# Kernel tuning notes

Measured on AMD Instinct MI355X. Metric: run time of the kernel, lower is better.

## Reference

```python
import jax, jax.numpy as jnp
import numpy as np

B, G, GS = 1024, 2000, 25   # batch, num gene groups, group size
H1, H2, C = 1024, 512, 10
EPS = 1e-5


def _xavier(key, shape, fan_in, fan_out):
    lim = np.sqrt(6.0 / (fan_in + fan_out))
    return jax.random.uniform(key, shape, jnp.float32, -lim, lim)


def setup_inputs() -> dict:
    key = jax.random.key(0)
    ks = jax.random.split(key, 8)
    x = jax.random.normal(ks[0], (B, G * GS), jnp.float32)
    # per-group Linear(GS, 1) weights stacked -> block-diagonal grouped GEMM
    gene_w = _xavier(ks[1], (G, GS), GS, 1)
    gene_b = jnp.zeros((G,), jnp.float32)
    W1 = _xavier(ks[2], (G, H1), G, H1)
    b1 = jnp.zeros((H1,), jnp.float32)
    W2 = _xavier(ks[3], (H1, H2), H1, H2)
    b2 = jnp.zeros((H2,), jnp.float32)
    Wout = _xavier(ks[4], (H2, C), H2, C)
    bout = jnp.zeros((C,), jnp.float32)
    Wres = _xavier(ks[5], (G, C), G, C)
    bres = jnp.zeros((C,), jnp.float32)
    gamma1 = jnp.ones((H1,), jnp.float32); beta1 = jnp.zeros((H1,), jnp.float32)
    gamma2 = jnp.ones((H2,), jnp.float32); beta2 = jnp.zeros((H2,), jnp.float32)
    return dict(x=x, gene_w=gene_w, gene_b=gene_b, W1=W1, b1=b1,
                gamma1=gamma1, beta1=beta1, W2=W2, b2=b2,
                gamma2=gamma2, beta2=beta2, Wout=Wout, bout=bout,
                Wres=Wres, bres=bres)


def _batch_norm(h, gamma, beta):
    # training-mode BatchNorm1d: biased batch statistics over axis 0
    mu = jnp.mean(h, axis=0)
    var = jnp.mean(jnp.square(h - mu), axis=0)
    return gamma * (h - mu) * jax.lax.rsqrt(var + EPS) + beta


def reference(x, gene_w, gene_b, W1, b1, gamma1, beta1, W2, b2,
              gamma2, beta2, Wout, bout, Wres, bres):
    # fused replacement for the per-group Linear(GS,1)+ReLU loop + cat
    xg = x.reshape(B, G, GS)
    g = jax.nn.relu(jnp.einsum('bgk,gk->bg', xg, gene_w) + gene_b)  # [B, G]
    h1 = jax.nn.relu(_batch_norm(g @ W1 + b1, gamma1, beta1))       # [B, H1]
    h2 = jax.nn.relu(_batch_norm(h1 @ W2 + b2, gamma2, beta2))      # [B, H2]
    x_main = h2 @ Wout + bout                                       # [B, C]
    x_res = g @ Wres + bres                                         # [B, C]
    return jax.nn.softmax(x_main + x_res, axis=1)
```

## Files before the change

kernel.cpp:

```cpp
#include <hip/hip_runtime.h>
#include <math.h>

#define NB   1024
#define NG   2000
#define NGS  25
#define KP   2048
#define NH1  1024
#define NH2  512
#define NC   10
#define EPSV 1e-5f
#define GPB  200
#define RB   8


typedef __attribute__((ext_vector_type(8)))  __bf16 bf16x8;
typedef __attribute__((ext_vector_type(4)))  float  f32x4;
typedef __attribute__((ext_vector_type(16))) float  f32x16;
typedef __attribute__((ext_vector_type(8)))  unsigned short u16x8;
typedef __attribute__((ext_vector_type(4)))  unsigned short u16x4;

__device__ __forceinline__ unsigned short f2bf(float f) {
  union { float f; unsigned u; } v; v.f = f;
  return (unsigned short)((v.u + 0x7fffu + ((v.u >> 16) & 1u)) >> 16);
}
__device__ __forceinline__ float bf2f(unsigned short b) {
  union { unsigned u; float f; } v; v.u = ((unsigned)b) << 16;
  return v.f;
}

__global__ __launch_bounds__(256) void prep_kernel(
    const float* __restrict__ x, const float* __restrict__ gw,
    const float* __restrict__ gb, unsigned short* __restrict__ g_bf,
    const float* __restrict__ W1, unsigned short* __restrict__ W1bT,
    const float* __restrict__ W2, unsigned short* __restrict__ W2bT,
    const float* __restrict__ Wres, float* __restrict__ rp,
    float* __restrict__ stats) {
  __shared__ __attribute__((aligned(16))) float xs[GPB * NGS];
  __shared__ __attribute__((aligned(16))) float ws[GPB * NC];
  __shared__ float rred[4][NC];
  int t = threadIdx.x;

  if (blockIdx.y < 10) {
    int blk = blockIdx.y;
    int b0 = blockIdx.x * RB;
    const float4* gsrc = (const float4*)(gw + (size_t)blk * (GPB * NGS));
    float4* xd = (float4*)xs;
    for (int i = t; i < (GPB * NGS) / 4; i += 256) xd[i] = gsrc[i];
    const float4* wsrc = (const float4*)(Wres + (size_t)blk * (GPB * NC));
    float4* wd = (float4*)ws;
    for (int i = t; i < (GPB * NC) / 4; i += 256) wd[i] = wsrc[i];
    __syncthreads();
    float gwr[NGS];
    float gbv = 0.f;
    int gi = blk * GPB + t;
    if (t < GPB) {
#pragma unroll
      for (int k = 0; k < NGS; ++k) gwr[k] = xs[t * NGS + k];
      gbv = gb[gi];
    }
    __syncthreads();
    int lane = t & 63, wave = t >> 6;
    for (int r = 0; r < RB; ++r) {
      int b = b0 + r;
      const float4* src = (const float4*)(x + (size_t)b * (NG * NGS) + blk * (GPB * NGS));
      for (int i = t; i < (GPB * NGS) / 4; i += 256) xd[i] = src[i];
      __syncthreads();
      float g = 0.f;
      if (t < GPB) {
        float acc = 0.f;
        const float* xp = xs + t * NGS;
#pragma unroll
        for (int k = 0; k < NGS; ++k) acc = fmaf(xp[k], gwr[k], acc);
        g = fmaxf(acc + gbv, 0.f);
        g_bf[(size_t)b * KP + gi] = f2bf(g);
      } else if (blk == 9 && t < GPB + (KP - NG)) {
        g_bf[(size_t)b * KP + NG + (t - GPB)] = 0;
      }
#pragma unroll
      for (int c = 0; c < NC; ++c) {
        float v = (t < GPB) ? g * ws[t * NC + c] : 0.f;
        for (int off = 32; off > 0; off >>= 1) v += __shfl_down(v, off, 64);
        if (lane == 0) rred[wave][c] = v;
      }
      __syncthreads();
      if (t < NC)
        rp[(size_t)b * (10 * NC) + blk * NC + t] =
            rred[0][t] + rred[1][t] + rred[2][t] + rred[3][t];
      __syncthreads();
    }
    return;
  }

  int px = (blockIdx.y - 10) * 128 + blockIdx.x;
  if (px == 640) {
    for (int i = t; i < 3072; i += 256) stats[i] = 0.f;
    return;
  }
  if (px > 640) return;
  const float* src; unsigned short* dst; int K, N, Kpad, k0, n0;
  if (px < 512)      { src = W1; dst = W1bT; K = NG;  N = NH1; Kpad = KP;
                       k0 = (px & 31) * 64; n0 = (px >> 5) * 64; }
  else               { int xi = px - 512;
                       src = W2; dst = W2bT; K = NH1; N = NH2; Kpad = NH1;
                       k0 = (xi & 15) * 64; n0 = (xi >> 4) * 64; }

  unsigned short (*ts)[72] = (unsigned short (*)[72])xs;
  int c4 = (t & 15) * 4;
  int r  = t >> 4;
  for (int rr = r; rr < 64; rr += 16) {
    int k = k0 + rr;
    float4 v = make_float4(0.f, 0.f, 0.f, 0.f);
    if (k < K) v = *(const float4*)&src[(size_t)k * N + n0 + c4];
    ts[rr][c4 + 0] = f2bf(v.x); ts[rr][c4 + 1] = f2bf(v.y);
    ts[rr][c4 + 2] = f2bf(v.z); ts[rr][c4 + 3] = f2bf(v.w);
  }
  __syncthreads();
  int rr8 = (t & 7) * 8;
  int cc  = t >> 3;
  for (int c = cc; c < 64; c += 32) {
    u16x8 val;
#pragma unroll
    for (int i = 0; i < 8; ++i) val[i] = ts[rr8 + i][c];
    *(u16x8*)&dst[(size_t)(n0 + c) * Kpad + k0 + rr8] = val;
  }
}

__global__ __launch_bounds__(256) void gemm1_kernel(
    const unsigned short* __restrict__ A,
    const unsigned short* __restrict__ Bt,
    float* __restrict__ C, float* __restrict__ sum, float* __restrict__ sq,
    int M, int N, int Kp) {
  __shared__ unsigned short As[32][68];
  __shared__ unsigned short Bs[64][68];
  __shared__ float ebuf[2 * 64 * 17];
  int t = threadIdx.x;
  int m0 = blockIdx.y * 32, n0 = blockIdx.x * 64;
  int wave = t >> 6, lane = t & 63;
  int h = wave & 1;
  int p = wave >> 1;
  int l31 = lane & 31, l5 = lane >> 5;
  int srow = t >> 3, skc = (t & 7) * 8;

  f32x16 acc;
#pragma unroll
  for (int q = 0; q < 16; ++q) acc[q] = 0.f;

  const unsigned short* Ap = A + (size_t)(m0 + srow) * Kp + skc;
  const unsigned short* Bp = Bt + (size_t)(n0 + srow) * Kp + skc;
  size_t rstep = 32 * (size_t)Kp;

  u16x8 pa0 = *(const u16x8*)(Ap);
  u16x8 pb0 = *(const u16x8*)(Bp);
  u16x8 pb1 = *(const u16x8*)(Bp + rstep);

  for (int k0 = 0; k0 < Kp; k0 += 64) {
    *(u16x8*)&As[srow][skc]      = pa0;
    *(u16x8*)&Bs[srow][skc]      = pb0;
    *(u16x8*)&Bs[srow + 32][skc] = pb1;
    __syncthreads();
    if (k0 + 64 < Kp) {
      pa0 = *(const u16x8*)(Ap + k0 + 64);
      pb0 = *(const u16x8*)(Bp + k0 + 64);
      pb1 = *(const u16x8*)(Bp + k0 + 64 + rstep);
    }
    int kb = p * 32 + l5 * 8;
    {
      bf16x8 av = *(const bf16x8*)&As[l31][kb];
      bf16x8 bv = *(const bf16x8*)&Bs[h * 32 + l31][kb];
      acc = __builtin_amdgcn_mfma_f32_32x32x16_bf16(av, bv, acc, 0, 0, 0);
    }
    {
      bf16x8 av = *(const bf16x8*)&As[l31][kb + 16];
      bf16x8 bv = *(const bf16x8*)&Bs[h * 32 + l31][kb + 16];
      acc = __builtin_amdgcn_mfma_f32_32x32x16_bf16(av, bv, acc, 0, 0, 0);
    }
    __syncthreads();
  }

  float* eb = ebuf + (size_t)(h * 64 + lane) * 17;
  if (p == 1) {
#pragma unroll
    for (int r = 0; r < 16; ++r) eb[r] = acc[r];
  }
  __syncthreads();
  if (p == 0) {
    float s = 0.f, ss = 0.f;
#pragma unroll
    for (int r = 0; r < 16; ++r) {
      float v = acc[r] + eb[r];
      int row = m0 + (r & 3) + 8 * (r >> 2) + 4 * l5;
      C[(size_t)row * N + n0 + h * 32 + l31] = v;
      s += v;
      ss = fmaf(v, v, ss);
    }
    s  += __shfl_down(s, 32, 64);
    ss += __shfl_down(ss, 32, 64);
    if (lane < 32) {
      atomicAdd(&sum[n0 + h * 32 + lane], s);
      atomicAdd(&sq[n0 + h * 32 + lane], ss);
    }
  }
}

__global__ __launch_bounds__(256) void gemm2_kernel(
    const float* __restrict__ A,
    const unsigned short* __restrict__ Bt,
    float* __restrict__ C, const float* __restrict__ sum1,
    const float* __restrict__ sq1, const float* __restrict__ gam1,
    const float* __restrict__ bet1, float* __restrict__ sum2,
    float* __restrict__ sq2, int M, int N, int Kp) {
  __shared__ unsigned short As[32][72];
  __shared__ unsigned short Bs[32][72];
  __shared__ float sc1s[NH1], sh1s[NH1];
  int t = threadIdx.x;
  int m0 = blockIdx.y * 32, n0 = blockIdx.x * 32;
  int wave = t >> 6, lane = t & 63;
  int wm = (wave >> 1) * 16, wn = (wave & 1) * 16;
  int fm = lane & 15, fk = (lane >> 4) * 8;
  int srow = t >> 3, skc = (t & 7) * 8;

  for (int k = t; k < Kp; k += 256) {
    float mu  = sum1[k] * (1.f / NB);
    float var = sq1[k] * (1.f / NB) - mu * mu;
    float scv = gam1[k] * rsqrtf(var + EPSV);
    sc1s[k] = scv;
    sh1s[k] = fmaf(-mu, scv, bet1[k]);
  }

  f32x4 acc = (f32x4){0.f, 0.f, 0.f, 0.f};

  const float* Ap = A + (size_t)(m0 + srow) * Kp + skc;
  const unsigned short* Bp = Bt + (size_t)(n0 + srow) * Kp + skc;

  f32x4 pa0 = *(const f32x4*)(Ap);
  f32x4 pa1 = *(const f32x4*)(Ap + 4);
  u16x8 pb0 = *(const u16x8*)(Bp);
  __syncthreads();

  for (int k0 = 0; k0 < Kp; k0 += 64) {
    f32x4 scl = *(const f32x4*)&sc1s[k0 + skc];
    f32x4 sch = *(const f32x4*)&sc1s[k0 + skc + 4];
    f32x4 shl = *(const f32x4*)&sh1s[k0 + skc];
    f32x4 shh = *(const f32x4*)&sh1s[k0 + skc + 4];
    u16x8 a0;
#pragma unroll
    for (int i = 0; i < 4; ++i) {
      a0[i]     = f2bf(fmaxf(fmaf(pa0[i], scl[i], shl[i]), 0.f));
      a0[i + 4] = f2bf(fmaxf(fmaf(pa1[i], sch[i], shh[i]), 0.f));
    }
    *(u16x8*)&As[srow][skc] = a0;
    *(u16x8*)&Bs[srow][skc] = pb0;
    __syncthreads();
    if (k0 + 64 < Kp) {
      pa0 = *(const f32x4*)(Ap + k0 + 64);
      pa1 = *(const f32x4*)(Ap + k0 + 64 + 4);
      pb0 = *(const u16x8*)(Bp + k0 + 64);
    }
#pragma unroll
    for (int s = 0; s < 2; ++s) {
      bf16x8 af = *(const bf16x8*)&As[wm + fm][s * 32 + fk];
      bf16x8 bf = *(const bf16x8*)&Bs[wn + fm][s * 32 + fk];
      acc = __builtin_amdgcn_mfma_f32_16x16x32_bf16(af, bf, acc, 0, 0, 0);
    }
    __syncthreads();
  }

  int crow = (lane >> 4) * 4, ccol = lane & 15;
  float s = 0.f, ss = 0.f;
#pragma unroll
  for (int r = 0; r < 4; ++r) {
    float v = acc[r];
    int m = m0 + wm + crow + r;
    int n = n0 + wn + ccol;
    C[(size_t)m * N + n] = v;
    s += v;
    ss = fmaf(v, v, ss);
  }
  s  += __shfl_down(s, 32, 64);  s  += __shfl_down(s, 16, 64);
  ss += __shfl_down(ss, 32, 64); ss += __shfl_down(ss, 16, 64);
  if (lane < 16) {
    atomicAdd(&sum2[n0 + wn + lane], s);
    atomicAdd(&sq2[n0 + wn + lane], ss);
  }
}

__global__ __launch_bounds__(256) void final_kernel(
    const float* __restrict__ t2, const float* __restrict__ sum2,
    const float* __restrict__ sq2, const float* __restrict__ gam2,
    const float* __restrict__ bet2, const float* __restrict__ rp,
    const float* __restrict__ Wout, const float* __restrict__ bout,
    const float* __restrict__ bres, float* __restrict__ out) {
  __shared__ __attribute__((aligned(16))) float wl[NH2 * NC];
  __shared__ float red[4][NC];
  __shared__ float logits[NC];
  int b = blockIdx.x;
  int t = threadIdx.x;

  const float4* wsrc = (const float4*)Wout;
  float4* wdst = (float4*)wl;
#pragma unroll
  for (int i = 0; i < (NH2 * NC / 4) / 256; ++i)
    wdst[t + i * 256] = wsrc[t + i * 256];
  __syncthreads();

  float acc[NC] = {};
#pragma unroll
  for (int half = 0; half < 2; ++half) {
    int h = t + half * 256;
    float raw = t2[(size_t)b * NH2 + h];
    float mu  = sum2[h] * (1.f / NB);
    float var = sq2[h] * (1.f / NB) - mu * mu;
    float scv = gam2[h] * rsqrtf(var + EPSV);
    float hr  = fmaxf(fmaf(raw, scv, fmaf(-mu, scv, bet2[h])), 0.f);
    const float* wrow = &wl[h * NC];
#pragma unroll
    for (int c = 0; c < NC; ++c) acc[c] = fmaf(hr, wrow[c], acc[c]);
  }

  int lane = t & 63, wave = t >> 6;
#pragma unroll
  for (int c = 0; c < NC; ++c) {
    float v = acc[c];
    for (int off = 32; off > 0; off >>= 1) v += __shfl_down(v, off, 64);
    if (lane == 0) red[wave][c] = v;
  }
  __syncthreads();
  if (t < NC) {
    float v = red[0][t] + red[1][t] + red[2][t] + red[3][t] + bout[t] + bres[t];
    const float* rpb = rp + (size_t)b * (10 * NC);
#pragma unroll
    for (int kb = 0; kb < 10; ++kb) v += rpb[kb * NC + t];
    logits[t] = v;
  }
  __syncthreads();
  if (t == 0) {
    float mx = logits[0];
#pragma unroll
    for (int c = 1; c < NC; ++c) mx = fmaxf(mx, logits[c]);
    float e[NC], s = 0.f;
#pragma unroll
    for (int c = 0; c < NC; ++c) { e[c] = expf(logits[c] - mx); s += e[c]; }
    float inv = 1.f / s;
#pragma unroll
    for (int c = 0; c < NC; ++c) out[(size_t)b * NC + c] = e[c] * inv;
  }
}

extern "C" void kernel_launch(void* const* d_in, const int* in_sizes, int n_in,
                              void* d_out, int out_size, void* d_ws, size_t ws_size,
                              hipStream_t stream) {
  const float* x      = (const float*)d_in[0];
  const float* gw     = (const float*)d_in[1];
  const float* gb     = (const float*)d_in[2];
  const float* W1     = (const float*)d_in[3];
  const float* gamma1 = (const float*)d_in[5];
  const float* beta1  = (const float*)d_in[6];
  const float* W2     = (const float*)d_in[7];
  const float* gamma2 = (const float*)d_in[9];
  const float* beta2  = (const float*)d_in[10];
  const float* Wout   = (const float*)d_in[11];
  const float* bout   = (const float*)d_in[12];
  const float* Wres   = (const float*)d_in[13];
  const float* bres   = (const float*)d_in[14];
  float* out = (float*)d_out;

  char* p = (char*)d_ws;
  unsigned short* g_bf = (unsigned short*)p; p += (size_t)NB * KP * 2;
  unsigned short* W1bT = (unsigned short*)p; p += (size_t)NH1 * KP * 2;
  unsigned short* W2bT = (unsigned short*)p; p += (size_t)NH2 * NH1 * 2;
  float* t1 = (float*)p; p += (size_t)NB * NH1 * 4;
  float* t2 = (float*)p; p += (size_t)NB * NH2 * 4;
  float* stats = (float*)p; p += 3072 * 4;
  float* rp = (float*)p; p += (size_t)NB * 10 * NC * 4;
  float* sum1 = stats, *sq1 = stats + 1024, *sum2 = stats + 2048, *sq2 = stats + 2560;

  prep_kernel<<<dim3(128, 16), 256, 0, stream>>>(x, gw, gb, g_bf,
                                                 W1, W1bT, W2, W2bT,
                                                 Wres, rp, stats);

  gemm1_kernel<<<dim3(NH1 / 64, NB / 32), 256, 0, stream>>>(
      g_bf, W1bT, t1, sum1, sq1, NB, NH1, KP);

  gemm2_kernel<<<dim3(NH2 / 32, NB / 32), 256, 0, stream>>>(
      t1, W2bT, t2, sum1, sq1, gamma1, beta1, sum2, sq2, NB, NH2, NH1);

  final_kernel<<<NB, 256, 0, stream>>>(t2, sum2, sq2, gamma2, beta2, rp,
                                       Wout, bout, bres, out);
}
```

Measured before the change: 360.5 us.

## Fold residual projection into GEMM1 as extra columns and double-buffer x loads

The residual projection g@Wres, previously done in prep_kernel with per-row shuffle reductions and partial sums, is now computed as an extra 64-column tile appended to the transposed bf16 W1 matrix, so gemm1 produces it with MFMA alongside the hidden layer. prep_kernel also prefetches the next x row into registers while computing the current one, and uses two LDS buffers to drop two barriers per row. This removes the reduction and sync overhead from the memory-bound prep stage. In exchange it adds one column tile of gemm1 work, and the residual path now runs in bf16 instead of fp32.

```diff
diff --git a/kernel.cpp b/kernel.cpp
--- a/kernel.cpp
+++ b/kernel.cpp
@@ -6,6 +6,7 @@
 #define NGS  25
 #define KP   2048
 #define NH1  1024
+#define NH1X 1088
 #define NH2  512
 #define NC   10
 #define EPSV 1e-5f
@@ -17,15 +18,10 @@
 typedef __attribute__((ext_vector_type(4)))  float  f32x4;
 typedef __attribute__((ext_vector_type(16))) float  f32x16;
 typedef __attribute__((ext_vector_type(8)))  unsigned short u16x8;
-typedef __attribute__((ext_vector_type(4)))  unsigned short u16x4;
 
 __device__ __forceinline__ unsigned short f2bf(float f) {
   union { float f; unsigned u; } v; v.f = f;
   return (unsigned short)((v.u + 0x7fffu + ((v.u >> 16) & 1u)) >> 16);
-}
-__device__ __forceinline__ float bf2f(unsigned short b) {
-  union { unsigned u; float f; } v; v.u = ((unsigned)b) << 16;
-  return v.f;
 }
 
 __global__ __launch_bounds__(256) void prep_kernel(
@@ -33,86 +29,109 @@
     const float* __restrict__ gb, unsigned short* __restrict__ g_bf,
     const float* __restrict__ W1, unsigned short* __restrict__ W1bT,
     const float* __restrict__ W2, unsigned short* __restrict__ W2bT,
-    const float* __restrict__ Wres, float* __restrict__ rp,
-    float* __restrict__ stats) {
-  __shared__ __attribute__((aligned(16))) float xs[GPB * NGS];
-  __shared__ __attribute__((aligned(16))) float ws[GPB * NC];
-  __shared__ float rred[4][NC];
+    const float* __restrict__ Wres, float* __restrict__ stats) {
+  __shared__ __attribute__((aligned(16))) float xs[2][GPB * NGS];
   int t = threadIdx.x;
 
   if (blockIdx.y < 10) {
     int blk = blockIdx.y;
     int b0 = blockIdx.x * RB;
-    const float4* gsrc = (const float4*)(gw + (size_t)blk * (GPB * NGS));
-    float4* xd = (float4*)xs;
-    for (int i = t; i < (GPB * NGS) / 4; i += 256) xd[i] = gsrc[i];
-    const float4* wsrc = (const float4*)(Wres + (size_t)blk * (GPB * NC));
-    float4* wd = (float4*)ws;
-    for (int i = t; i < (GPB * NC) / 4; i += 256) wd[i] = wsrc[i];
+    const size_t chunk_off = (size_t)blk * (GPB * NGS);
+
+    float4 st[5];
+#pragma unroll
+    for (int j = 0; j < 5; ++j) st[j] = make_float4(0.f, 0.f, 0.f, 0.f);
+    {
+      const float4* s0 = (const float4*)(x + (size_t)b0 * (NG * NGS) + chunk_off);
+#pragma unroll
+      for (int j = 0; j < 5; ++j) {
+        int i = t + j * 256;
+        if (i < (GPB * NGS) / 4) st[j] = s0[i];
+      }
+    }
+    const float4* gsrc = (const float4*)(gw + chunk_off);
+    float4* xd0 = (float4*)xs[0];
+    for (int i = t; i < (GPB * NGS) / 4; i += 256) xd0[i] = gsrc[i];
     __syncthreads();
     float gwr[NGS];
     float gbv = 0.f;
     int gi = blk * GPB + t;
     if (t < GPB) {
 #pragma unroll
-      for (int k = 0; k < NGS; ++k) gwr[k] = xs[t * NGS + k];
+      for (int k = 0; k < NGS; ++k) gwr[k] = xs[0][t * NGS + k];
       gbv = gb[gi];
     }
     __syncthreads();
-    int lane = t & 63, wave = t >> 6;
+
     for (int r = 0; r < RB; ++r) {
+      float* xc = xs[r & 1];
+      float4* xdc = (float4*)xc;
+#pragma unroll
+      for (int j = 0; j < 5; ++j) {
+        int i = t + j * 256;
+        if (i < (GPB * NGS) / 4) xdc[i] = st[j];
+      }
+      __syncthreads();
+      if (r + 1 < RB) {
+        const float4* sn = (const float4*)
+            (x + (size_t)(b0 + r + 1) * (NG * NGS) + chunk_off);
+#pragma unroll
+        for (int j = 0; j < 5; ++j) {
+          int i = t + j * 256;
+          if (i < (GPB * NGS) / 4) st[j] = sn[i];
+        }
+      }
       int b = b0 + r;
-      const float4* src = (const float4*)(x + (size_t)b * (NG * NGS) + blk * (GPB * NGS));
-      for (int i = t; i < (GPB * NGS) / 4; i += 256) xd[i] = src[i];
-      __syncthreads();
-      float g = 0.f;
       if (t < GPB) {
         float acc = 0.f;
-        const float* xp = xs + t * NGS;
+        const float* xp = xc + t * NGS;
 #pragma unroll
         for (int k = 0; k < NGS; ++k) acc = fmaf(xp[k], gwr[k], acc);
-        g = fmaxf(acc + gbv, 0.f);
-        g_bf[(size_t)b * KP + gi] = f2bf(g);
+        g_bf[(size_t)b * KP + gi] = f2bf(fmaxf(acc + gbv, 0.f));
       } else if (blk == 9 && t < GPB + (KP - NG)) {
         g_bf[(size_t)b * KP + NG + (t - GPB)] = 0;
       }
-#pragma unroll
-      for (int c = 0; c < NC; ++c) {
-        float v = (t < GPB) ? g * ws[t * NC + c] : 0.f;
-        for (int off = 32; off > 0; off >>= 1) v += __shfl_down(v, off, 64);
-        if (lane == 0) rred[wave][c] = v;
-      }
-      __syncthreads();
-      if (t < NC)
-        rp[(size_t)b * (10 * NC) + blk * NC + t] =
-            rred[0][t] + rred[1][t] + rred[2][t] + rred[3][t];
-      __syncthreads();
     }
     return;
   }
 
   int px = (blockIdx.y - 10) * 128 + blockIdx.x;
-  if (px == 640) {
+  if (px == 672) {
     for (int i = t; i < 3072; i += 256) stats[i] = 0.f;
     return;
   }
-  if (px > 640) return;
+  if (px > 672) return;
   const float* src; unsigned short* dst; int K, N, Kpad, k0, n0;
+  int wres_mode = 0;
   if (px < 512)      { src = W1; dst = W1bT; K = NG;  N = NH1; Kpad = KP;
                        k0 = (px & 31) * 64; n0 = (px >> 5) * 64; }
-  else               { int xi = px - 512;
+  else if (px < 640) { int xi = px - 512;
                        src = W2; dst = W2bT; K = NH1; N = NH2; Kpad = NH1;
                        k0 = (xi & 15) * 64; n0 = (xi >> 4) * 64; }
+  else               { int xi = px - 640;
+                       src = Wres; dst = W1bT; K = NG; N = NC; Kpad = KP;
+                       k0 = xi * 64; n0 = 1024; wres_mode = 1; }
 
   unsigned short (*ts)[72] = (unsigned short (*)[72])xs;
   int c4 = (t & 15) * 4;
   int r  = t >> 4;
   for (int rr = r; rr < 64; rr += 16) {
     int k = k0 + rr;
-    float4 v = make_float4(0.f, 0.f, 0.f, 0.f);
-    if (k < K) v = *(const float4*)&src[(size_t)k * N + n0 + c4];
-    ts[rr][c4 + 0] = f2bf(v.x); ts[rr][c4 + 1] = f2bf(v.y);
-    ts[rr][c4 + 2] = f2bf(v.z); ts[rr][c4 + 3] = f2bf(v.w);
+    float v[4] = {0.f, 0.f, 0.f, 0.f};
+    if (!wres_mode) {
+      if (k < K) {
+        float4 q = *(const float4*)&src[(size_t)k * N + n0 + c4];
+        v[0] = q.x; v[1] = q.y; v[2] = q.z; v[3] = q.w;
+      }
+    } else {
+      if (k < K) {
+#pragma unroll
+        for (int i = 0; i < 4; ++i)
+          if (c4 + i < NC) v[i] = src[(size_t)k * NC + c4 + i];
+      }
+    }
+    ts[rr][c4 + 0] = f2bf(v[0]); ts[rr][c4 + 1] = f2bf(v[1]);
+    ts[rr][c4 + 2] = f2bf(v[2]); ts[rr][c4 + 3] = f2bf(v[3]);
   }
   __syncthreads();
   int rr8 = (t & 7) * 8;
@@ -129,7 +148,7 @@
     const unsigned short* __restrict__ A,
     const unsigned short* __restrict__ Bt,
     float* __restrict__ C, float* __restrict__ sum, float* __restrict__ sq,
-    int M, int N, int Kp) {
+    float* __restrict__ rpx, int M, int N, int Kp) {
   __shared__ unsigned short As[32][68];
   __shared__ unsigned short Bs[64][68];
   __shared__ float ebuf[2 * 64 * 17];
@@ -189,15 +208,21 @@
     for (int r = 0; r < 16; ++r) {
       float v = acc[r] + eb[r];
       int row = m0 + (r & 3) + 8 * (r >> 2) + 4 * l5;
-      C[(size_t)row * N + n0 + h * 32 + l31] = v;
-      s += v;
-      ss = fmaf(v, v, ss);
-    }
-    s  += __shfl_down(s, 32, 64);
-    ss += __shfl_down(ss, 32, 64);
-    if (lane < 32) {
-      atomicAdd(&sum[n0 + h * 32 + lane], s);
-      atomicAdd(&sq[n0 + h * 32 + lane], ss);
+      if (n0 < N) {
+        C[(size_t)row * N + n0 + h * 32 + l31] = v;
+        s += v;
+        ss = fmaf(v, v, ss);
+      } else {
+        rpx[(size_t)row * 64 + h * 32 + l31] = v;
+      }
+    }
+    if (n0 < N) {
+      s  += __shfl_down(s, 32, 64);
+      ss += __shfl_down(ss, 32, 64);
+      if (lane < 32) {
+        atomicAdd(&sum[n0 + h * 32 + lane], s);
+        atomicAdd(&sq[n0 + h * 32 + lane], ss);
+      }
     }
   }
 }
@@ -287,7 +312,7 @@
 __global__ __launch_bounds__(256) void final_kernel(
     const float* __restrict__ t2, const float* __restrict__ sum2,
     const float* __restrict__ sq2, const float* __restrict__ gam2,
-    const float* __restrict__ bet2, const float* __restrict__ rp,
+    const float* __restrict__ bet2, const float* __restrict__ rpx,
     const float* __restrict__ Wout, const float* __restrict__ bout,
     const float* __restrict__ bres, float* __restrict__ out) {
   __shared__ __attribute__((aligned(16))) float wl[NH2 * NC];
@@ -326,11 +351,8 @@
   }
   __syncthreads();
   if (t < NC) {
-    float v = red[0][t] + red[1][t] + red[2][t] + red[3][t] + bout[t] + bres[t];
-    const float* rpb = rp + (size_t)b * (10 * NC);
-#pragma unroll
-    for (int kb = 0; kb < 10; ++kb) v += rpb[kb * NC + t];
-    logits[t] = v;
+    logits[t] = red[0][t] + red[1][t] + red[2][t] + red[3][t] +
+                bout[t] + bres[t] + rpx[(size_t)b * 64 + t];
   }
   __syncthreads();
   if (t == 0) {
@@ -366,24 +388,24 @@
 
   char* p = (char*)d_ws;
   unsigned short* g_bf = (unsigned short*)p; p += (size_t)NB * KP * 2;
-  unsigned short* W1bT = (unsigned short*)p; p += (size_t)NH1 * KP * 2;
+  unsigned short* W1bT = (unsigned short*)p; p += (size_t)NH1X * KP * 2;
   unsigned short* W2bT = (unsigned short*)p; p += (size_t)NH2 * NH1 * 2;
   float* t1 = (float*)p; p += (size_t)NB * NH1 * 4;
   float* t2 = (float*)p; p += (size_t)NB * NH2 * 4;
   float* stats = (float*)p; p += 3072 * 4;
-  float* rp = (float*)p; p += (size_t)NB * 10 * NC * 4;
+  float* rpx = (float*)p; p += (size_t)NB * 64 * 4;
   float* sum1 = stats, *sq1 = stats + 1024, *sum2 = stats + 2048, *sq2 = stats + 2560;
 
   prep_kernel<<<dim3(128, 16), 256, 0, stream>>>(x, gw, gb, g_bf,
                                                  W1, W1bT, W2, W2bT,
-                                                 Wres, rp, stats);
-
-  gemm1_kernel<<<dim3(NH1 / 64, NB / 32), 256, 0, stream>>>(
-      g_bf, W1bT, t1, sum1, sq1, NB, NH1, KP);
+                                                 Wres, stats);
+
+  gemm1_kernel<<<dim3(NH1X / 64, NB / 32), 256, 0, stream>>>(
+      g_bf, W1bT, t1, sum1, sq1, rpx, NB, NH1, KP);
 
   gemm2_kernel<<<dim3(NH2 / 32, NB / 32), 256, 0, stream>>>(
       t1, W2bT, t2, sum1, sq1, gamma1, beta1, sum2, sq2, NB, NH2, NH1);
 
-  final_kernel<<<NB, 256, 0, stream>>>(t2, sum2, sq2, gamma2, beta2, rp,
+  final_kernel<<<NB, 256, 0, stream>>>(t2, sum2, sq2, gamma2, beta2, rpx,
                                        Wout, bout, bres, out);
 }
```

New measurement: 359.8 us. Within noise of the previous version (-0.2%).
